# Kernel optimization log

Hardware: AMD Instinct MI355X
Metric: run time of the kernel (lower is better)

Reference implementation:

```python
import jax, jax.numpy as jnp
import numpy as np

G, T, E, D, C = 4, 2048, 8, 1024, 2048
CAP_FACTORS = (0.25, 0.25, 0.125, 0.125, 0.0625, 0.0625, 0.0625, 0.0625)


def setup_inputs() -> dict:
    key = jax.random.key(0)
    k1, k2 = jax.random.split(key, 2)
    token_inputs = jax.random.normal(k1, (G, T, D), dtype=jnp.float32)
    # RouterWeights: Linear(dim -> num_experts), weight ~ N(0, 0.02), bias = 0
    W = jax.random.normal(k2, (E, D), dtype=jnp.float32) * 0.02
    b = jnp.zeros((E,), dtype=jnp.float32)
    return {"token_inputs": token_inputs, "W": W, "b": b,
            "num_experts": E, "expert_capacity": C}


def reference(token_inputs, W, b, num_experts, expert_capacity):
    # router logits [G, T, E] (jitter_noise = 0, no padding mask)
    logits = jnp.einsum('gtd,ed->gte', token_inputs, W) + b
    probs = jax.nn.softmax(logits, axis=-1)

    caps = [max(1, int(f * expert_capacity)) for f in CAP_FACTORS]
    tokens = token_inputs.shape[1]

    disp_parts, comb_parts = [], []
    for i, cap in enumerate(caps):  # fixed small loop over experts
        # each expert chooses its top-`cap` tokens
        gate, idx = jax.lax.top_k(probs[:, :, i], cap)        # [G, cap]
        onehot = jax.nn.one_hot(idx, tokens, dtype=jnp.int32)  # [G, cap, T]
        d = jnp.transpose(onehot, (0, 2, 1))                   # [G, T, cap]
        c = gate[:, None, :] * d.astype(probs.dtype)           # [G, T, cap]
        pad = expert_capacity - cap
        disp_parts.append(jnp.pad(d, ((0, 0), (0, 0), (0, pad))))
        comb_parts.append(jnp.pad(c, ((0, 0), (0, 0), (0, pad))))

    dispatch_mask = jnp.stack(disp_parts, axis=2)   # [G, T, E, C] int32
    combine_array = jnp.stack(comb_parts, axis=2)   # [G, T, E, C] float32

    router_z_loss = jnp.mean(jnp.square(jax.nn.log_softmax(logits, axis=-1)))
    return dispatch_mask, combine_array, router_z_loss
```

## Files before the change

kernel.cpp:

```cpp
#include <hip/hip_runtime.h>

#define GG 4
#define TT 2048
#define EE 8
#define DD 1024
#define CC 2048

static constexpr long long GTEC = (long long)GG * TT * EE * CC;
static constexpr int NROW = GG * TT * EE;
static constexpr int NBLK_A = GG * TT / 4;

typedef float vf4 __attribute__((ext_vector_type(4)));

static constexpr int WS_PROBS = 0;
static constexpr int WS_SEL   = 65536;
static constexpr int WS_ZPART = 196608;

__global__ __launch_bounds__(256) void router_probs_kernel(
    const float* __restrict__ x, const float* __restrict__ W,
    const float* __restrict__ bias, float* __restrict__ probs,
    float* __restrict__ zpart)
{
    __shared__ float sW[EE * DD];
    __shared__ float zsh[4];
    {
        const vf4* W4 = (const vf4*)W;
        vf4* sW4 = (vf4*)sW;
        for (int i = threadIdx.x; i < EE * DD / 4; i += 256) sW4[i] = W4[i];
    }
    __syncthreads();

    const int wave = threadIdx.x >> 6;
    const int lane = threadIdx.x & 63;
    const int token = blockIdx.x * 4 + wave;
    const vf4* xr4 = (const vf4*)(x + (long long)token * DD);
    const vf4* sW4 = (const vf4*)sW;

    float acc[EE];
#pragma unroll
    for (int e = 0; e < EE; ++e) acc[e] = 0.f;

#pragma unroll
    for (int it = 0; it < 4; ++it) {
        const int k4 = lane + 64 * it;
        const vf4 xv = xr4[k4];
#pragma unroll
        for (int e = 0; e < EE; ++e) {
            const vf4 wv = sW4[e * (DD / 4) + k4];
            acc[e] = fmaf(xv.x, wv.x, acc[e]);
            acc[e] = fmaf(xv.y, wv.y, acc[e]);
            acc[e] = fmaf(xv.z, wv.z, acc[e]);
            acc[e] = fmaf(xv.w, wv.w, acc[e]);
        }
    }

#pragma unroll
    for (int off = 32; off > 0; off >>= 1) {
#pragma unroll
        for (int e = 0; e < EE; ++e)
            acc[e] += __shfl_xor(acc[e], off, 64);
    }

#pragma unroll
    for (int e = 0; e < EE; ++e) acc[e] += bias[e];

    float m = acc[0];
#pragma unroll
    for (int e = 1; e < EE; ++e) m = fmaxf(m, acc[e]);
    float s = 0.f;
#pragma unroll
    for (int e = 0; e < EE; ++e) s += expf(acc[e] - m);
    const float lse = m + logf(s);

    if (lane < EE)
        probs[(long long)token * EE + lane] = expf(acc[lane] - lse);

    if (lane == 0) {
        float zs = 0.f;
#pragma unroll
        for (int e = 0; e < EE; ++e) {
            const float d = acc[e] - lse;
            zs = fmaf(d, d, zs);
        }
        zsh[wave] = zs;
    }
    __syncthreads();
    if (threadIdx.x == 0)
        zpart[blockIdx.x] = (zsh[0] + zsh[1]) + (zsh[2] + zsh[3]);
}

__global__ __launch_bounds__(1024) void topk_select_kernel(
    const float* __restrict__ probs, unsigned long long* __restrict__ sel)
{
    __shared__ unsigned long long keys[TT];
    const int g = blockIdx.x >> 3;
    const int e = blockIdx.x & 7;
    const int caps[EE] = {512, 512, 256, 256, 128, 128, 128, 128};
    const int cap = caps[e];
    const int base = (g * EE + e) * TT;

    for (int t = threadIdx.x; t < TT; t += 1024) {
        const float p = probs[((long long)g * TT + t) * EE + e];
        const unsigned int pb = __float_as_uint(p);
        keys[t] = ((unsigned long long)pb << 32) |
                  (unsigned long long)(0xFFFFFFFFu - (unsigned)t);
    }
    __syncthreads();

    for (int k = 2; k <= TT; k <<= 1) {
        for (int j = k >> 1; j > 0; j >>= 1) {
            for (int v = threadIdx.x; v < TT; v += 1024) {
                const int ixj = v ^ j;
                if (ixj > v) {
                    const bool desc = ((v & k) == 0);
                    const unsigned long long a = keys[v];
                    const unsigned long long b = keys[ixj];
                    if (desc ? (a < b) : (a > b)) { keys[v] = b; keys[ixj] = a; }
                }
            }
            __syncthreads();
        }
    }

    for (int i = threadIdx.x; i < TT; i += 1024) {
        const unsigned long long kk = keys[i];
        const int t = (int)(0xFFFFFFFFu - (unsigned)(kk & 0xFFFFFFFFull));
        const unsigned int pb = (unsigned int)(kk >> 32);
        const unsigned int rank1 = (i < cap) ? (unsigned int)(i + 1) : 0u;
        sel[base + t] = ((unsigned long long)pb << 32) | (unsigned long long)rank1;
    }
}

__global__ __launch_bounds__(256) void fill_outputs_kernel(
    const unsigned long long* __restrict__ sel,
    const float* __restrict__ zpart, float* __restrict__ out)
{
    const int wid  = (int)((blockIdx.x * 256 + threadIdx.x) >> 6);
    const int lane = threadIdx.x & 63;

    const int e = wid & (EE - 1);
    const int t = (wid >> 3) & (TT - 1);
    const int g = wid >> 14;

    const unsigned long long sv = sel[(g * EE + e) * TT + t];
    const unsigned int rank1 = (unsigned int)(sv & 0xFFFFFFFFull);
    const float gate = __uint_as_float((unsigned int)(sv >> 32));
    const int cq = ((int)rank1 - 1) >> 2;
    const int cr = ((int)rank1 - 1) & 3;

    vf4* drow = (vf4*)out + (long long)wid * (CC / 4);
    vf4* crow = (vf4*)(out + GTEC) + (long long)wid * (CC / 4);

#pragma unroll
    for (int j0 = 0; j0 < CC / 4; j0 += 64) {
        const int j = j0 + lane;
        vf4 vd = (vf4)(0.f);
        vf4 vc = (vf4)(0.f);
        if (rank1 && j == cq) {
            vd[cr] = 1.0f;
            vc[cr] = gate;
        }
        __builtin_nontemporal_store(vd, &drow[j]);
        __builtin_nontemporal_store(vc, &crow[j]);
    }

    if (blockIdx.x == 0 && threadIdx.x < 64) {
        float zs = 0.f;
        for (int i = lane; i < NBLK_A; i += 64) zs += zpart[i];
#pragma unroll
        for (int off = 32; off > 0; off >>= 1)
            zs += __shfl_xor(zs, off, 64);
        if (lane == 0)
            out[2 * GTEC] = zs * (1.0f / ((float)GG * TT * EE));
    }
}

extern "C" void kernel_launch(void* const* d_in, const int* in_sizes, int n_in,
                              void* d_out, int out_size, void* d_ws, size_t ws_size,
                              hipStream_t stream) {
    const float* x    = (const float*)d_in[0];
    const float* W    = (const float*)d_in[1];
    const float* bias = (const float*)d_in[2];
    float* out = (float*)d_out;
    float* ws  = (float*)d_ws;

    float* probs = ws + WS_PROBS;
    unsigned long long* sel = (unsigned long long*)(ws + WS_SEL);
    float* zpart = ws + WS_ZPART;

    router_probs_kernel<<<NBLK_A, 256, 0, stream>>>(x, W, bias, probs, zpart);
    topk_select_kernel<<<GG * EE, 1024, 0, stream>>>(probs, sel);
    fill_outputs_kernel<<<NROW / 4, 256, 0, stream>>>(sel, zpart, out);
}
```

Baseline: 1.119 ms.

## Replace dense output fill kernel with memset plus sparse scatter from top-k

Drops the per-row fill kernel that wrote every zero and one-hot entry of both output tensors. The whole output is now cleared with hipMemsetAsync, and the top-k kernel scatters only the selected (one, gate) pairs directly into the outputs. The z-loss reduction moves into the top-k kernel, and the intermediate selection buffer goes away. This relies on the memset reaching write bandwidth comparable to the custom nontemporal store kernel, and it adds an extra stream operation.

After: 1.089 ms. -2.7%, faster.

```diff
diff --git a/kernel.cpp b/kernel.cpp
--- a/kernel.cpp
+++ b/kernel.cpp
@@ -7,14 +7,12 @@
 #define CC 2048
 
 static constexpr long long GTEC = (long long)GG * TT * EE * CC;
-static constexpr int NROW = GG * TT * EE;
 static constexpr int NBLK_A = GG * TT / 4;
 
 typedef float vf4 __attribute__((ext_vector_type(4)));
 
 static constexpr int WS_PROBS = 0;
-static constexpr int WS_SEL   = 65536;
-static constexpr int WS_ZPART = 196608;
+static constexpr int WS_ZPART = 65536;
 
 __global__ __launch_bounds__(256) void router_probs_kernel(
     const float* __restrict__ x, const float* __restrict__ W,
@@ -89,15 +87,26 @@
         zpart[blockIdx.x] = (zsh[0] + zsh[1]) + (zsh[2] + zsh[3]);
 }
 
-__global__ __launch_bounds__(1024) void topk_select_kernel(
-    const float* __restrict__ probs, unsigned long long* __restrict__ sel)
+__global__ __launch_bounds__(1024) void topk_scatter_kernel(
+    const float* __restrict__ probs, const float* __restrict__ zpart,
+    float* __restrict__ out)
 {
     __shared__ unsigned long long keys[TT];
     const int g = blockIdx.x >> 3;
     const int e = blockIdx.x & 7;
     const int caps[EE] = {512, 512, 256, 256, 128, 128, 128, 128};
     const int cap = caps[e];
-    const int base = (g * EE + e) * TT;
+
+    if (blockIdx.x == 0 && threadIdx.x < 64) {
+        const int lane = threadIdx.x;
+        float zs = 0.f;
+        for (int i = lane; i < NBLK_A; i += 64) zs += zpart[i];
+#pragma unroll
+        for (int off = 32; off > 0; off >>= 1)
+            zs += __shfl_xor(zs, off, 64);
+        if (lane == 0)
+            out[2 * GTEC] = zs * (1.0f / ((float)GG * TT * EE));
+    }
 
     for (int t = threadIdx.x; t < TT; t += 1024) {
         const float p = probs[((long long)g * TT + t) * EE + e];
@@ -122,56 +131,14 @@
         }
     }
 
-    for (int i = threadIdx.x; i < TT; i += 1024) {
-        const unsigned long long kk = keys[i];
+    if (threadIdx.x < cap) {
+        const unsigned long long kk = keys[threadIdx.x];
         const int t = (int)(0xFFFFFFFFu - (unsigned)(kk & 0xFFFFFFFFull));
-        const unsigned int pb = (unsigned int)(kk >> 32);
-        const unsigned int rank1 = (i < cap) ? (unsigned int)(i + 1) : 0u;
-        sel[base + t] = ((unsigned long long)pb << 32) | (unsigned long long)rank1;
-    }
-}
-
-__global__ __launch_bounds__(256) void fill_outputs_kernel(
-    const unsigned long long* __restrict__ sel,
-    const float* __restrict__ zpart, float* __restrict__ out)
-{
-    const int wid  = (int)((blockIdx.x * 256 + threadIdx.x) >> 6);
-    const int lane = threadIdx.x & 63;
-
-    const int e = wid & (EE - 1);
-    const int t = (wid >> 3) & (TT - 1);
-    const int g = wid >> 14;
-
-    const unsigned long long sv = sel[(g * EE + e) * TT + t];
-    const unsigned int rank1 = (unsigned int)(sv & 0xFFFFFFFFull);
-    const float gate = __uint_as_float((unsigned int)(sv >> 32));
-    const int cq = ((int)rank1 - 1) >> 2;
-    const int cr = ((int)rank1 - 1) & 3;
-
-    vf4* drow = (vf4*)out + (long long)wid * (CC / 4);
-    vf4* crow = (vf4*)(out + GTEC) + (long long)wid * (CC / 4);
-
-#pragma unroll
-    for (int j0 = 0; j0 < CC / 4; j0 += 64) {
-        const int j = j0 + lane;
-        vf4 vd = (vf4)(0.f);
-        vf4 vc = (vf4)(0.f);
-        if (rank1 && j == cq) {
-            vd[cr] = 1.0f;
-            vc[cr] = gate;
-        }
-        __builtin_nontemporal_store(vd, &drow[j]);
-        __builtin_nontemporal_store(vc, &crow[j]);
-    }
-
-    if (blockIdx.x == 0 && threadIdx.x < 64) {
-        float zs = 0.f;
-        for (int i = lane; i < NBLK_A; i += 64) zs += zpart[i];
-#pragma unroll
-        for (int off = 32; off > 0; off >>= 1)
-            zs += __shfl_xor(zs, off, 64);
-        if (lane == 0)
-            out[2 * GTEC] = zs * (1.0f / ((float)GG * TT * EE));
+        const float gate = __uint_as_float((unsigned int)(kk >> 32));
+        const long long base =
+            (((long long)g * TT + t) * EE + e) * CC + threadIdx.x;
+        out[base] = 1.0f;
+        out[GTEC + base] = gate;
     }
 }
 
@@ -185,10 +152,11 @@
     float* ws  = (float*)d_ws;
 
     float* probs = ws + WS_PROBS;
-    unsigned long long* sel = (unsigned long long*)(ws + WS_SEL);
     float* zpart = ws + WS_ZPART;
 
+    hipMemsetAsync(d_out, 0, (size_t)out_size * sizeof(float), stream);
+
     router_probs_kernel<<<NBLK_A, 256, 0, stream>>>(x, W, bias, probs, zpart);
-    topk_select_kernel<<<GG * EE, 1024, 0, stream>>>(probs, sel);
-    fill_outputs_kernel<<<NROW / 4, 256, 0, stream>>>(sel, zpart, out);
+
+    topk_scatter_kernel<<<GG * EE, 1024, 0, stream>>>(probs, zpart, out);
 }
```
